# Optimization experiments

Measured on AMD Instinct MI355X. Metric: run time of the kernel, lower is better.

## Reference

```python
import jax, jax.numpy as jnp
import numpy as np

D_IN, D_HIDDEN, DT_RANK = 768, 16, 48


def setup_inputs() -> dict:
    key = jax.random.key(0)
    ks = jax.random.split(key, 6)
    b, l, d, n, r = 2, 2048, D_IN, D_HIDDEN, DT_RANK
    p = 3 * n + 2 * d + 2 * r  # x_proj output width = 1680
    x = jax.random.normal(ks[0], (b, l, d), jnp.float32)
    z = jax.random.normal(ks[1], (b, d, l), jnp.float32)
    # A_log = log(repeat(arange(1, n+1), 'n -> d n'))
    A_log = jnp.log(jnp.broadcast_to(jnp.arange(1, n + 1, dtype=jnp.float32), (d, n)))
    D = jnp.ones((d,), jnp.float32)
    W_xproj = jax.random.normal(ks[2], (p, d), jnp.float32) / np.sqrt(d)
    W_dt = jax.random.normal(ks[3], (d, r), jnp.float32) / np.sqrt(r)
    # dt bias init: inverse-softplus of dt ~ LogUniform(1e-3, 1e-1)
    dt = jnp.exp(jax.random.uniform(ks[4], (d,)) * (np.log(0.1) - np.log(0.001)) + np.log(0.001))
    dt = jnp.clip(dt, 1e-4)
    b_dt = dt + jnp.log(-jnp.expm1(-dt))
    return dict(x=x, z=z, A_log=A_log, D=D, W_xproj=W_xproj, W_dt=W_dt, b_dt=b_dt)


def reference(x, z, A_log, D, W_xproj, W_dt, b_dt):
    b, l, d = x.shape
    n = A_log.shape[1]
    r = W_dt.shape[1]
    A = -jnp.exp(A_log)                      # (d, n)
    proj = x @ W_xproj.T                     # (b, l, 3n + 2d + 2r)
    Bm = proj[..., :n]                       # (b, l, n)  input matrix B
    Cm = proj[..., 2 * n:3 * n]              # (b, l, n)  output matrix C
    dt = proj[..., 3 * n + 2 * d:3 * n + 2 * d + r]   # (b, l, r)
    # NOTE: source adds dt_proj bias via the Linear AND again via delta_bias -> 2*b_dt
    delta = jax.nn.softplus(dt @ W_dt.T + 2.0 * b_dt)  # (b, l, d)
    dA = jnp.exp(delta[..., None] * A)                  # (b, l, d, n)
    dBu = (delta * x)[..., None] * Bm[:, :, None, :]    # (b, l, d, n)

    def step(h, inp):
        dA_t, dBu_t, C_t = inp
        h = dA_t * h + dBu_t                 # (b, d, n)
        return h, jnp.einsum('bdn,bn->bd', h, C_t)

    h0 = jnp.zeros((b, d, n), x.dtype)
    _, ys = jax.lax.scan(step, h0, (jnp.swapaxes(dA, 0, 1), jnp.swapaxes(dBu, 0, 1), jnp.swapaxes(Cm, 0, 1)))
    y = jnp.swapaxes(ys, 0, 1) + x * D       # (b, l, d)  + skip D*u
    zl = jnp.swapaxes(z, 1, 2)               # z is (b, d, l) -> (b, l, d)
    return y * (zl * jax.nn.sigmoid(zl))     # gate with silu(z)
```

## Files before the change

### kernel.cpp

```cpp
#include <hip/hip_runtime.h>
#include <math.h>

#define BATCH 2
#define LSEQ  2048
#define DIM   768
#define NST   16
#define RDT   48
#define BL    (BATCH*LSEQ)
#define NCHUNK 32
#define CLEN   (LSEQ/NCHUNK)
#define CPAD   68
#define NPACK  (CLEN/4)
#define LP4    (LSEQ/4)
#define L2E    1.4426950408889634f

typedef __attribute__((ext_vector_type(8))) short short8;
typedef __attribute__((ext_vector_type(4))) float float4e;

__device__ __forceinline__ ushort f2bf(float f) {
    union { float f; unsigned u; } v; v.f = f;
    unsigned u = v.u;
    u += 0x7fffu + ((u >> 16) & 1u);
    return (ushort)(u >> 16);
}

template <int CTRL>
__device__ __forceinline__ float dpp_add(float v) {
    const int s = __builtin_amdgcn_update_dpp(__float_as_int(v), __float_as_int(v),
                                              CTRL, 0xF, 0xF, false);
    return v + __int_as_float(s);
}

__device__ __forceinline__ short8 cvt8(float4 a, float4 b) {
    short8 r;
    r[0] = (short)f2bf(a.x); r[1] = (short)f2bf(a.y);
    r[2] = (short)f2bf(a.z); r[3] = (short)f2bf(a.w);
    r[4] = (short)f2bf(b.x); r[5] = (short)f2bf(b.y);
    r[6] = (short)f2bf(b.z); r[7] = (short)f2bf(b.w);
    return r;
}

__global__ __launch_bounds__(320) void proj_gemm_kernel(
        const float* __restrict__ x, const float* __restrict__ Wx,
        const float* __restrict__ Wdt, const float* __restrict__ bdt,
        float* __restrict__ Bpk, float* __restrict__ Cpk,
        float* __restrict__ deltaT, float* __restrict__ xT) {
    __shared__ float dtp_s[16 * 65];
    const int m0   = blockIdx.x * 16;
    const int nt   = threadIdx.x >> 6;
    const int lane = threadIdx.x & 63;
    const int col  = lane & 15;
    const int quad = lane >> 4;
    const int b  = m0 >> 11;
    const int t0 = m0 & 2047;

    for (int i = threadIdx.x; i < 16 * 65; i += 320) dtp_s[i] = 0.f;
    __syncthreads();

    const int j80  = nt * 16 + col;
    const int wrow = (j80 < 16) ? j80 : ((j80 < 32) ? (j80 + 16) : (j80 + 1552));
    const float* A  = x + (size_t)(m0 + col) * DIM + quad * 8;
    const float* Wr = Wx + (size_t)wrow * DIM + quad * 8;

    const int kklo = nt * 5;
    const int kkhi = (nt == 4) ? 24 : (kklo + 5);

    float4e acc = {};
    #pragma unroll 4
    for (int kk = 0; kk < 24; ++kk) {
        const float4 a0 = *(const float4*)(A + kk * 32);
        const float4 a1 = *(const float4*)(A + kk * 32 + 4);
        if (kk >= kklo && kk < kkhi) {
            const int dbase = kk * 32 + quad * 8;
            float* xc = xT + ((size_t)(b * DIM + dbase)) * LSEQ + t0 + col;
            xc[0 * LSEQ] = a0.x; xc[1 * LSEQ] = a0.y;
            xc[2 * LSEQ] = a0.z; xc[3 * LSEQ] = a0.w;
            xc[4 * LSEQ] = a1.x; xc[5 * LSEQ] = a1.y;
            xc[6 * LSEQ] = a1.z; xc[7 * LSEQ] = a1.w;
        }
        const float4 w0 = *(const float4*)(Wr + kk * 32);
        const float4 w1 = *(const float4*)(Wr + kk * 32 + 4);
        acc = __builtin_amdgcn_mfma_f32_16x16x32_bf16(cvt8(a0, a1), cvt8(w0, w1),
                                                      acc, 0, 0, 0);
    }

    if (nt == 0) {
        ((float4*)Bpk)[((size_t)(b * LP4 + (t0 >> 2) + quad)) * NST + col] = *(float4*)&acc;
    } else if (nt == 1) {
        ((float4*)Cpk)[((size_t)(b * LP4 + (t0 >> 2) + quad)) * NST + col] = *(float4*)&acc;
    } else {
        #pragma unroll
        for (int r = 0; r < 4; ++r)
            dtp_s[(quad * 4 + r) * 65 + (nt - 2) * 16 + col] = acc[r];
    }
    __syncthreads();

    short8 da0, da1;
    #pragma unroll
    for (int j = 0; j < 8; ++j) {
        da0[j] = (short)f2bf(dtp_s[col * 65 + quad * 8 + j]);
        da1[j] = (short)f2bf(dtp_s[col * 65 + 32 + quad * 8 + j]);
    }
    for (int dt = nt; dt < 48; dt += 5) {
        const int d0 = dt * 16;
        const float* wd = Wdt + (size_t)(d0 + col) * RDT;
        const short8 b0 = cvt8(*(const float4*)(wd + quad * 8),
                               *(const float4*)(wd + quad * 8 + 4));
        short8 b1 = {};
        if (quad < 2)
            b1 = cvt8(*(const float4*)(wd + 32 + quad * 8),
                      *(const float4*)(wd + 32 + quad * 8 + 4));
        float4e dacc = {};
        dacc = __builtin_amdgcn_mfma_f32_16x16x32_bf16(da0, b0, dacc, 0, 0, 0);
        dacc = __builtin_amdgcn_mfma_f32_16x16x32_bf16(da1, b1, dacc, 0, 0, 0);
        const float bb = 2.0f * bdt[d0 + col];
        float4 sp;
        {
            const float v0 = dacc[0] + bb, v1 = dacc[1] + bb;
            const float v2 = dacc[2] + bb, v3 = dacc[3] + bb;
            sp.x = (v0 > 20.f) ? v0 : __logf(1.f + __expf(v0));
            sp.y = (v1 > 20.f) ? v1 : __logf(1.f + __expf(v1));
            sp.z = (v2 > 20.f) ? v2 : __logf(1.f + __expf(v2));
            sp.w = (v3 > 20.f) ? v3 : __logf(1.f + __expf(v3));
        }
        *(float4*)(deltaT + ((size_t)(b * DIM + d0 + col)) * LSEQ + t0 + quad * 4) = sp;
    }
}

__global__ __launch_bounds__(512) void scan_kernel(
        const float* __restrict__ xT, const float* __restrict__ A_log,
        const float* __restrict__ Dp,
        const float* __restrict__ Bpk, const float* __restrict__ Cpk,
        const float* __restrict__ deltaT, float* __restrict__ yv) {
    __shared__ float sdel[NCHUNK * CPAD];
    __shared__ float sdlx[NCHUNK * CPAD];
    __shared__ float sP[NCHUNK][NST];
    __shared__ float sq[NCHUNK][NST];

    const int tid = threadIdx.x;
    const int ch = blockIdx.x;
    const int b = ch / DIM;
    const int d = ch % DIM;
    const size_t row = (size_t)ch * LSEQ;

    {
        const float4 dv4 = ((const float4*)(deltaT + row))[tid];
        const float4 xv4 = ((const float4*)(xT + row))[tid];
        const int sidx = (tid >> 4) * (CPAD / 4) + (tid & 15);
        ((float4*)sdel)[sidx] = dv4;
        ((float4*)sdlx)[sidx] = make_float4(dv4.x * xv4.x, dv4.y * xv4.y,
                                            dv4.z * xv4.z, dv4.w * xv4.w);
    }
    __syncthreads();

    const int g = tid >> 4;
    const int n = tid & 15;
    const float Aln2 = -__expf(A_log[d * NST + n]) * L2E;
    const float4* Bg = (const float4*)Bpk + ((size_t)(b * LP4 + g * NPACK) * NST + n);
    const float4* Cg = (const float4*)Cpk + ((size_t)(b * LP4 + g * NPACK) * NST + n);
    const float4* xr = (const float4*)(xT + row) + g * NPACK;
    const float* dchunk = sdel + g * CPAD;
    const float* uchunk = sdlx + g * CPAD;

    {
        float h = 0.f, Ptot = 1.f;
        float4 Bn_ = Bg[0];
        #pragma unroll 4
        for (int p = 0; p < NPACK; ++p) {
            const float4 B4 = Bn_;
            if (p < NPACK - 1) Bn_ = Bg[(p + 1) * NST];
            const float4 dl = *(const float4*)(dchunk + 4 * p);
            const float4 ux = *(const float4*)(uchunk + 4 * p);
            const float u0 = ux.x * B4.x, u1 = ux.y * B4.y;
            const float u2 = ux.z * B4.z, u3 = ux.w * B4.w;
            const float e0  = __builtin_amdgcn_exp2f(Aln2 * dl.x);
            const float dA1 = __builtin_amdgcn_exp2f(Aln2 * dl.y);
            const float dA2 = __builtin_amdgcn_exp2f(Aln2 * dl.z);
            const float dA3 = __builtin_amdgcn_exp2f(Aln2 * dl.w);
            float s = u0;
            s = fmaf(dA1, s, u1); s = fmaf(dA2, s, u2); s = fmaf(dA3, s, u3);
            const float E3 = ((e0 * dA1) * (dA2 * dA3));
            h = fmaf(E3, h, s);
            Ptot *= E3;
        }
        sP[g][n] = Ptot;
        sq[g][n] = h;
    }
    __syncthreads();

    {
        float Pc = sP[g][n], qc = sq[g][n];
        #pragma unroll
        for (int s = 1; s < NCHUNK; s <<= 1) {
            float Pp = 1.f, qp = 0.f;
            if (g >= s) { Pp = sP[g - s][n]; qp = sq[g - s][n]; }
            __syncthreads();
            qc = fmaf(Pc, qp, qc);
            Pc *= Pp;
            sP[g][n] = Pc; sq[g][n] = qc;
            __syncthreads();
        }
    }

    {
        float h = (g == 0) ? 0.f : sq[g - 1][n];
        const float Dd = Dp[d];
        float4 Bn_ = Bg[0], Cn_ = Cg[0], xn_ = xr[0];
        #pragma unroll 4
        for (int p = 0; p < NPACK; ++p) {
            const float4 B4 = Bn_, C4 = Cn_, x4 = xn_;
            if (p < NPACK - 1) { Bn_ = Bg[(p + 1) * NST]; Cn_ = Cg[(p + 1) * NST]; xn_ = xr[p + 1]; }
            const float4 dl = *(const float4*)(dchunk + 4 * p);
            const float4 ux = *(const float4*)(uchunk + 4 * p);
            const float u0 = ux.x * B4.x, u1 = ux.y * B4.y;
            const float u2 = ux.z * B4.z, u3 = ux.w * B4.w;
            const float E0  = __builtin_amdgcn_exp2f(Aln2 * dl.x);
            const float dA1 = __builtin_amdgcn_exp2f(Aln2 * dl.y);
            const float dA2 = __builtin_amdgcn_exp2f(Aln2 * dl.z);
            const float dA3 = __builtin_amdgcn_exp2f(Aln2 * dl.w);
            const float E1 = E0 * dA1, E2 = E1 * dA2, E3 = E2 * dA3;
            const float s0 = u0;
            const float s1 = fmaf(dA1, s0, u1);
            const float s2 = fmaf(dA2, s1, u2);
            const float s3 = fmaf(dA3, s2, u3);
            const float h0 = fmaf(E0, h, s0);
            const float h1 = fmaf(E1, h, s1);
            const float h2 = fmaf(E2, h, s2);
            const float h3 = fmaf(E3, h, s3);
            h = h3;
            float p0 = h0 * C4.x, p1 = h1 * C4.y, p2 = h2 * C4.z, p3 = h3 * C4.w;
            p0 = dpp_add<0xB1>(p0); p0 = dpp_add<0x4E>(p0);
            p1 = dpp_add<0xB1>(p1); p1 = dpp_add<0x4E>(p1);
            p2 = dpp_add<0xB1>(p2); p2 = dpp_add<0x4E>(p2);
            p3 = dpp_add<0xB1>(p3); p3 = dpp_add<0x4E>(p3);
            float v = (n & 1) ? ((n & 2) ? p3 : p1) : ((n & 2) ? p2 : p0);
            v = dpp_add<0x124>(v);
            v = dpp_add<0x128>(v);
            if (n < 4) {
                const float xc = (n == 0) ? x4.x : (n == 1) ? x4.y : (n == 2) ? x4.z : x4.w;
                yv[row + g * CLEN + 4 * p + n] = fmaf(xc, Dd, v);
            }
        }
    }
}

__global__ __launch_bounds__(256) void xpose_out_kernel(
        const float* __restrict__ yv, const float* __restrict__ z,
        float* __restrict__ out) {
    __shared__ float tile[64 * 65];
    const int r0 = blockIdx.x * 64;
    const int c0 = blockIdx.y * 64;
    const int b  = blockIdx.z;
    const int tid = threadIdx.x;
    {
        const int c4 = tid & 15, rb = tid >> 4;
        #pragma unroll
        for (int rr = 0; rr < 4; ++rr) {
            const int row = rr * 16 + rb;
            const size_t gidx = ((size_t)b * DIM + r0 + row) * LSEQ + c0 + c4 * 4;
            const float4 v = *(const float4*)(yv + gidx);
            const float4 zv = *(const float4*)(z + gidx);
            tile[(c4 * 4 + 0) * 65 + row] = v.x * zv.x / (1.f + __expf(-zv.x));
            tile[(c4 * 4 + 1) * 65 + row] = v.y * zv.y / (1.f + __expf(-zv.y));
            tile[(c4 * 4 + 2) * 65 + row] = v.z * zv.z / (1.f + __expf(-zv.z));
            tile[(c4 * 4 + 3) * 65 + row] = v.w * zv.w / (1.f + __expf(-zv.w));
        }
    }
    __syncthreads();
    {
        const int t4 = tid & 15, dq = tid >> 4;
        #pragma unroll
        for (int pass = 0; pass < 4; ++pass) {
            const int ll = pass * 16 + dq;
            float4 v;
            v.x = tile[ll * 65 + t4 * 4 + 0];
            v.y = tile[ll * 65 + t4 * 4 + 1];
            v.z = tile[ll * 65 + t4 * 4 + 2];
            v.w = tile[ll * 65 + t4 * 4 + 3];
            *(float4*)(out + ((size_t)b * LSEQ + c0 + ll) * DIM + r0 + t4 * 4) = v;
        }
    }
}

extern "C" void kernel_launch(void* const* d_in, const int* in_sizes, int n_in,
                              void* d_out, int out_size, void* d_ws, size_t ws_size,
                              hipStream_t stream) {
    const float* x     = (const float*)d_in[0];
    const float* z     = (const float*)d_in[1];
    const float* A_log = (const float*)d_in[2];
    const float* D     = (const float*)d_in[3];
    const float* Wx    = (const float*)d_in[4];
    const float* Wdt   = (const float*)d_in[5];
    const float* bdt   = (const float*)d_in[6];
    float* out = (float*)d_out;

    float* ws     = (float*)d_ws;
    float* Bpk    = ws;
    float* Cpk    = Bpk + (size_t)BATCH * LP4 * NST * 4;
    float* deltaT = Cpk + (size_t)BATCH * LP4 * NST * 4;
    float* xT     = deltaT + (size_t)BATCH * DIM * LSEQ;
    float* yv     = xT;

    hipLaunchKernelGGL(proj_gemm_kernel, dim3(BL / 16), dim3(320), 0, stream,
                       x, Wx, Wdt, bdt, Bpk, Cpk, deltaT, xT);
    hipLaunchKernelGGL(scan_kernel, dim3(BATCH * DIM), dim3(512), 0, stream,
                       xT, A_log, D, Bpk, Cpk, deltaT, yv);
    hipLaunchKernelGGL(xpose_out_kernel, dim3(DIM / 64, LSEQ / 64, BATCH), dim3(256), 0, stream,
                       yv, z, out);
}
```

Baseline: 147.6 us.

## Split projection GEMM K-loop across two wave halves and pack bf16 via perm

The projection kernel doubles its block to 640 threads. Each group of five waves computes half of the K reduction, and the partial accumulators are combined through shared memory before B/C/dt are written. The delta projection loop is spread over all ten waves. The float-to-bf16 conversion is replaced by an add-and-byte-permute packing that rounds half-up instead of round-to-nearest-even. This is meant to shorten the serial MFMA chain and raise memory parallelism, at the cost of an extra barrier, shared-memory reduction traffic and slightly different rounding.

```diff
diff --git a/kernel.cpp b/kernel.cpp
--- a/kernel.cpp
+++ b/kernel.cpp
@@ -17,11 +17,18 @@
 typedef __attribute__((ext_vector_type(8))) short short8;
 typedef __attribute__((ext_vector_type(4))) float float4e;
 
-__device__ __forceinline__ ushort f2bf(float f) {
-    union { float f; unsigned u; } v; v.f = f;
-    unsigned u = v.u;
-    u += 0x7fffu + ((u >> 16) & 1u);
-    return (ushort)(u >> 16);
+__device__ __forceinline__ unsigned bfpk(float a, float b) {
+    const unsigned ua = __float_as_uint(a) + 0x8000u;
+    const unsigned ub = __float_as_uint(b) + 0x8000u;
+    return __builtin_amdgcn_perm(ub, ua, 0x07060302u);
+}
+__device__ __forceinline__ short8 pk8(float4 a, float4 b) {
+    union { unsigned u[4]; short8 s; } r;
+    r.u[0] = bfpk(a.x, a.y);
+    r.u[1] = bfpk(a.z, a.w);
+    r.u[2] = bfpk(b.x, b.y);
+    r.u[3] = bfpk(b.z, b.w);
+    return r.s;
 }
 
 template <int CTRL>
@@ -31,30 +38,24 @@
     return v + __int_as_float(s);
 }
 
-__device__ __forceinline__ short8 cvt8(float4 a, float4 b) {
-    short8 r;
-    r[0] = (short)f2bf(a.x); r[1] = (short)f2bf(a.y);
-    r[2] = (short)f2bf(a.z); r[3] = (short)f2bf(a.w);
-    r[4] = (short)f2bf(b.x); r[5] = (short)f2bf(b.y);
-    r[6] = (short)f2bf(b.z); r[7] = (short)f2bf(b.w);
-    return r;
-}
-
-__global__ __launch_bounds__(320) void proj_gemm_kernel(
+__global__ __launch_bounds__(640) void proj_gemm_kernel(
         const float* __restrict__ x, const float* __restrict__ Wx,
         const float* __restrict__ Wdt, const float* __restrict__ bdt,
         float* __restrict__ Bpk, float* __restrict__ Cpk,
         float* __restrict__ deltaT, float* __restrict__ xT) {
     __shared__ float dtp_s[16 * 65];
+    __shared__ float4 red_s[5 * 64];
     const int m0   = blockIdx.x * 16;
-    const int nt   = threadIdx.x >> 6;
+    const int w    = threadIdx.x >> 6;
+    const int half = (w >= 5) ? 1 : 0;
+    const int nt   = w - half * 5;
     const int lane = threadIdx.x & 63;
     const int col  = lane & 15;
     const int quad = lane >> 4;
     const int b  = m0 >> 11;
     const int t0 = m0 & 2047;
 
-    for (int i = threadIdx.x; i < 16 * 65; i += 320) dtp_s[i] = 0.f;
+    for (int i = threadIdx.x; i < 16 * 65; i += 640) dtp_s[i] = 0.f;
     __syncthreads();
 
     const int j80  = nt * 16 + col;
@@ -62,12 +63,14 @@
     const float* A  = x + (size_t)(m0 + col) * DIM + quad * 8;
     const float* Wr = Wx + (size_t)wrow * DIM + quad * 8;
 
-    const int kklo = nt * 5;
-    const int kkhi = (nt == 4) ? 24 : (kklo + 5);
+    const int kbase = half * 12;
+    const int kklo  = kbase + (nt * 12) / 5;
+    const int kkhi  = kbase + ((nt + 1) * 12) / 5;
 
     float4e acc = {};
     #pragma unroll 4
-    for (int kk = 0; kk < 24; ++kk) {
+    for (int kk2 = 0; kk2 < 12; ++kk2) {
+        const int kk = kbase + kk2;
         const float4 a0 = *(const float4*)(A + kk * 32);
         const float4 a1 = *(const float4*)(A + kk * 32 + 4);
         if (kk >= kklo && kk < kkhi) {
@@ -80,36 +83,51 @@
         }
         const float4 w0 = *(const float4*)(Wr + kk * 32);
         const float4 w1 = *(const float4*)(Wr + kk * 32 + 4);
-        acc = __builtin_amdgcn_mfma_f32_16x16x32_bf16(cvt8(a0, a1), cvt8(w0, w1),
+        acc = __builtin_amdgcn_mfma_f32_16x16x32_bf16(pk8(a0, a1), pk8(w0, w1),
                                                       acc, 0, 0, 0);
     }
 
-    if (nt == 0) {
-        ((float4*)Bpk)[((size_t)(b * LP4 + (t0 >> 2) + quad)) * NST + col] = *(float4*)&acc;
-    } else if (nt == 1) {
-        ((float4*)Cpk)[((size_t)(b * LP4 + (t0 >> 2) + quad)) * NST + col] = *(float4*)&acc;
-    } else {
+    if (half) {
+        red_s[nt * 64 + lane] = make_float4(acc[0], acc[1], acc[2], acc[3]);
+    }
+    __syncthreads();
+    if (!half) {
+        const float4 o = red_s[nt * 64 + lane];
+        acc[0] += o.x; acc[1] += o.y; acc[2] += o.z; acc[3] += o.w;
+        if (nt == 0) {
+            ((float4*)Bpk)[((size_t)(b * LP4 + (t0 >> 2) + quad)) * NST + col] = *(float4*)&acc;
+        } else if (nt == 1) {
+            ((float4*)Cpk)[((size_t)(b * LP4 + (t0 >> 2) + quad)) * NST + col] = *(float4*)&acc;
+        } else {
+            #pragma unroll
+            for (int r = 0; r < 4; ++r)
+                dtp_s[(quad * 4 + r) * 65 + (nt - 2) * 16 + col] = acc[r];
+        }
+    }
+    __syncthreads();
+
+    short8 da0, da1;
+    {
+        union { unsigned u[4]; short8 s; } r0, r1;
+        const float* base = dtp_s + col * 65 + quad * 8;
         #pragma unroll
-        for (int r = 0; r < 4; ++r)
-            dtp_s[(quad * 4 + r) * 65 + (nt - 2) * 16 + col] = acc[r];
-    }
-    __syncthreads();
-
-    short8 da0, da1;
-    #pragma unroll
-    for (int j = 0; j < 8; ++j) {
-        da0[j] = (short)f2bf(dtp_s[col * 65 + quad * 8 + j]);
-        da1[j] = (short)f2bf(dtp_s[col * 65 + 32 + quad * 8 + j]);
-    }
-    for (int dt = nt; dt < 48; dt += 5) {
+        for (int j = 0; j < 2; ++j) {
+            r0.u[2 * j]     = bfpk(base[4 * j], base[4 * j + 1]);
+            r0.u[2 * j + 1] = bfpk(base[4 * j + 2], base[4 * j + 3]);
+            r1.u[2 * j]     = bfpk(base[32 + 4 * j], base[32 + 4 * j + 1]);
+            r1.u[2 * j + 1] = bfpk(base[32 + 4 * j + 2], base[32 + 4 * j + 3]);
+        }
+        da0 = r0.s; da1 = r1.s;
+    }
+    for (int dt = w; dt < 48; dt += 10) {
         const int d0 = dt * 16;
         const float* wd = Wdt + (size_t)(d0 + col) * RDT;
-        const short8 b0 = cvt8(*(const float4*)(wd + quad * 8),
-                               *(const float4*)(wd + quad * 8 + 4));
+        const short8 b0 = pk8(*(const float4*)(wd + quad * 8),
+                              *(const float4*)(wd + quad * 8 + 4));
         short8 b1 = {};
         if (quad < 2)
-            b1 = cvt8(*(const float4*)(wd + 32 + quad * 8),
-                      *(const float4*)(wd + 32 + quad * 8 + 4));
+            b1 = pk8(*(const float4*)(wd + 32 + quad * 8),
+                     *(const float4*)(wd + 32 + quad * 8 + 4));
         float4e dacc = {};
         dacc = __builtin_amdgcn_mfma_f32_16x16x32_bf16(da0, b0, dacc, 0, 0, 0);
         dacc = __builtin_amdgcn_mfma_f32_16x16x32_bf16(da1, b1, dacc, 0, 0, 0);
@@ -301,7 +319,7 @@
     float* xT     = deltaT + (size_t)BATCH * DIM * LSEQ;
     float* yv     = xT;
 
-    hipLaunchKernelGGL(proj_gemm_kernel, dim3(BL / 16), dim3(320), 0, stream,
+    hipLaunchKernelGGL(proj_gemm_kernel, dim3(BL / 16), dim3(640), 0, stream,
                        x, Wx, Wdt, bdt, Bpk, Cpk, deltaT, xT);
     hipLaunchKernelGGL(scan_kernel, dim3(BATCH * DIM), dim3(512), 0, stream,
                        xT, A_log, D, Bpk, Cpk, deltaT, yv);
```

Result: faster. 144.6 us (-2.1%).
